# Performance work log

Hardware: AMD Instinct MI355X
Metric: run time of the kernel (lower is better)

## Reference

```python
import jax, jax.numpy as jnp
import numpy as np

ALPHA = 0.25
GAMMA = 2.0
HUBER_DELTA = 0.5  # init kwarg delta
REG_BETA = 1.0 / 9.0


def calc_iou(a, b):
    # a: [A,4] anchors, b: [M,4] gt boxes, xyxy
    area = (b[:, 2] - b[:, 0]) * (b[:, 3] - b[:, 1])  # [M]
    iw = jnp.clip(jnp.minimum(a[:, 2:3], b[:, 2]) - jnp.maximum(a[:, 0:1], b[:, 0]), 0.0)
    ih = jnp.clip(jnp.minimum(a[:, 3:4], b[:, 3]) - jnp.maximum(a[:, 1:2], b[:, 1]), 0.0)
    ua = jnp.clip(((a[:, 2] - a[:, 0]) * (a[:, 3] - a[:, 1]))[:, None] + area - iw * ih, 1e-8)
    return iw * ih / ua  # [A,M]


def _per_sample(cls, reg, dist, ann, anchor):
    # cls [A,C], reg [A,4], dist [A,1], ann [M,6], anchor [A,4]
    aw = anchor[:, 2] - anchor[:, 0]
    ah = anchor[:, 3] - anchor[:, 1]
    acx = anchor[:, 0] + 0.5 * aw
    acy = anchor[:, 1] + 0.5 * ah

    valid = ann[:, 4] != -1.0  # padding annotations have class == -1
    cls = jnp.clip(cls, 1e-4, 1.0 - 1e-4)

    iou = jnp.where(valid[None, :], calc_iou(anchor, ann[:, :4]), -1.0)  # [A,M]
    iou_max = iou.max(axis=1)
    iou_arg = iou.argmax(axis=1)
    assigned = ann[iou_arg]  # [A,6]

    pos = iou_max >= 0.5
    num_pos = pos.sum()
    denom = jnp.maximum(num_pos.astype(cls.dtype), 1.0)

    labels = assigned[:, 4].astype(jnp.int32)
    onehot = jax.nn.one_hot(labels, cls.shape[1], dtype=cls.dtype)
    # -1 = ignore, 0 = negative (IoU<0.4 or positive-but-not-this-class), 1 = assigned class
    targets = jnp.where(pos[:, None], onehot,
                        jnp.where((iou_max < 0.4)[:, None], 0.0, -1.0))

    af = jnp.where(targets == 1.0, ALPHA, 1.0 - ALPHA)
    fw = af * jnp.where(targets == 1.0, 1.0 - cls, cls) ** GAMMA
    bce = -(targets * jnp.log(cls) + (1.0 - targets) * jnp.log(1.0 - cls))
    cls_loss = jnp.where(targets != -1.0, fw * bce, 0.0).sum() / denom

    # empty-annotation fallback: all anchors treated as background
    cls_loss_empty = ((1.0 - ALPHA) * cls ** GAMMA * (-jnp.log(1.0 - cls))).sum()
    has_ann = valid.any()
    cls_loss = jnp.where(has_ann, cls_loss, cls_loss_empty)

    gw_raw = assigned[:, 2] - assigned[:, 0]
    gh_raw = assigned[:, 3] - assigned[:, 1]
    gcx = assigned[:, 0] + 0.5 * gw_raw  # centers use unclamped w/h (as in torch code)
    gcy = assigned[:, 1] + 0.5 * gh_raw
    gw = jnp.clip(gw_raw, 1.0)
    gh = jnp.clip(gh_raw, 1.0)
    t = jnp.stack([(gcx - acx) / aw, (gcy - acy) / ah,
                   jnp.log(gw / aw), jnp.log(gh / ah)], axis=1)
    t = t / jnp.asarray([0.1, 0.1, 0.2, 0.2], dtype=cls.dtype)
    diff = jnp.abs(t - reg)
    rl = jnp.where(diff <= REG_BETA, 0.5 * 9.0 * diff ** 2, diff - 0.5 / 9.0)
    posf = pos.astype(cls.dtype)
    reg_loss = jnp.where(num_pos > 0, (rl * posf[:, None]).sum() / (denom * 4.0), 0.0)

    # --- distance Huber loss (delta=0.5), positives only ---
    d = jnp.abs(dist[:, 0] - assigned[:, 5])
    hl = jnp.where(d <= HUBER_DELTA, 0.5 * d ** 2, HUBER_DELTA * (d - 0.5 * HUBER_DELTA))
    dist_loss = jnp.where(num_pos > 0, (hl * posf).sum() / denom, 0.0)

    return cls_loss, reg_loss, dist_loss


def reference(classifications, regressions, distances, anchors, annotations):
    anchor = anchors[0]
    cl, rl, dl = jax.vmap(_per_sample, in_axes=(0, 0, 0, 0, None))(
        classifications, regressions, distances, annotations, anchor)
    return (jnp.mean(cl, keepdims=True),
            jnp.mean(rl, keepdims=True),
            jnp.mean(dl, keepdims=True))


def setup_inputs() -> dict:
    key = jax.random.key(0)
    ks = jax.random.split(key, 10)
    B, A, C, M = 8, 120000, 80, 32
    IMG = 800.0

    classifications = jax.random.uniform(ks[0], (B, A, C), dtype=jnp.float32)
    regressions = jax.random.normal(ks[1], (B, A, 4), dtype=jnp.float32)
    distances = jax.random.normal(ks[2], (B, A, 1), dtype=jnp.float32) * 10.0 + 50.0

    # anchors: valid xyxy boxes over an 800px image
    acx = jax.random.uniform(ks[3], (A,), minval=0.0, maxval=IMG)
    acy = jax.random.uniform(ks[4], (A,), minval=0.0, maxval=IMG)
    aw = jax.random.uniform(ks[5], (A, 2), minval=16.0, maxval=256.0)
    anchors = jnp.stack([acx - 0.5 * aw[:, 0], acy - 0.5 * aw[:, 1],
                         acx + 0.5 * aw[:, 0], acy + 0.5 * aw[:, 1]], axis=1)[None].astype(jnp.float32)

    # annotations: [B,M,6] = x1,y1,x2,y2,class,distance (all valid)
    gc = jax.random.uniform(ks[6], (B, M, 2), minval=100.0, maxval=IMG - 100.0)
    gs = jax.random.uniform(ks[7], (B, M, 2), minval=32.0, maxval=300.0)
    boxes = jnp.concatenate([gc - 0.5 * gs, gc + 0.5 * gs], axis=-1)
    labels = jax.random.randint(ks[8], (B, M, 1), 0, C).astype(jnp.float32)
    gdist = jax.random.uniform(ks[9], (B, M, 1), minval=1.0, maxval=100.0)
    annotations = jnp.concatenate([boxes, labels, gdist], axis=-1).astype(jnp.float32)

    return {"classifications": classifications, "regressions": regressions,
            "distances": distances, "anchors": anchors, "annotations": annotations}
```

## Files before the change

### kernel.cpp

```cpp
#include <hip/hip_runtime.h>
#include <hip/hip_bf16.h>


typedef float v4f __attribute__((ext_vector_type(4)));

#define LN2_075 0.51986038542f

__device__ __forceinline__ float wave_reduce_sum(float v) {
#pragma unroll
    for (int off = 32; off > 0; off >>= 1) v += __shfl_down(v, off);
    return v;
}

__device__ __forceinline__ float smooth_l1(float d) {
    return d <= (1.0f / 9.0f) ? 4.5f * d * d : d - (0.5f / 9.0f);
}

template <int CPA>
__global__ __launch_bounds__(256) void fused_kernel(
    const float* __restrict__ cls, const float* __restrict__ reg,
    const float* __restrict__ dist, const float* __restrict__ anchors,
    const float* __restrict__ ann, float4* __restrict__ partials,
    int A, int M, int nb) {
    const int b = blockIdx.y;
    const int base = blockIdx.x << 8;
    const int tid = threadIdx.x;
    const int lane = tid & 63;

    __shared__ float s_ann[64 * 6];
    const float* annb = ann + (size_t)b * M * 6;
    for (int i = tid; i < M * 6; i += 256) s_ann[i] = annb[i];

    const v4f* __restrict__ clsb = (const v4f*)(cls + ((size_t)b * A + base) * (CPA * 4));
    float acc2 = 0.f;
    if (base + 256 <= A) {
#pragma unroll
        for (int k = 0; k < CPA; ++k) {
            const v4f cv = __builtin_nontemporal_load(&clsb[k * 256 + tid]);
#pragma unroll
            for (int j = 0; j < 4; ++j) {
                const float c = fminf(fmaxf(cv[j], 1e-4f), 1.0f - 1e-4f);
                acc2 = fmaf(c * c, __log2f(1.0f - c), acc2);
            }
        }
    } else {
        const int nch = (A - base) * CPA;
        for (int k = 0; k < CPA; ++k) {
            const int idx = k * 256 + tid;
            if (idx < nch) {
                const v4f cv = __builtin_nontemporal_load(&clsb[idx]);
#pragma unroll
                for (int j = 0; j < 4; ++j) {
                    const float c = fminf(fmaxf(cv[j], 1e-4f), 1.0f - 1e-4f);
                    acc2 = fmaf(c * c, __log2f(1.0f - c), acc2);
                }
            }
        }
    }

    __syncthreads();

    const int a = base + tid;
    float l_npos = 0.f, l_reg = 0.f, l_dist = 0.f;
    int st = -1;
    if (a < A) {
        const float4 av = *(const float4*)(anchors + (size_t)a * 4);
        const float aw = av.z - av.x, ah = av.w - av.y;
        const float acx = av.x + 0.5f * aw, acy = av.y + 0.5f * ah;
        const float aarea = aw * ah;

        float best = -1.0f;
        int bi = 0;
        for (int m = 0; m < M; ++m) {
            const float* g = s_ann + m * 6;
            float iou = -1.0f;
            if (g[4] != -1.0f) {
                float iw = fmaxf(fminf(av.z, g[2]) - fmaxf(av.x, g[0]), 0.f);
                float ih = fmaxf(fminf(av.w, g[3]) - fmaxf(av.y, g[1]), 0.f);
                float inter = iw * ih;
                float area = (g[2] - g[0]) * (g[3] - g[1]);
                float ua = fmaxf(aarea + area - inter, 1e-8f);
                iou = inter / ua;
            }
            if (iou > best) { best = iou; bi = m; }
        }

        if (best >= 0.5f) {
            const float* g = s_ann + bi * 6;
            st = (int)g[4];
            l_npos = 1.f;
            const float4 rv = *(const float4*)(reg + ((size_t)b * A + a) * 4);
            const float gwr = g[2] - g[0], ghr = g[3] - g[1];
            const float gcx = g[0] + 0.5f * gwr, gcy = g[1] + 0.5f * ghr;
            const float gw = fmaxf(gwr, 1.f), gh = fmaxf(ghr, 1.f);
            const float t0 = ((gcx - acx) / aw) / 0.1f;
            const float t1 = ((gcy - acy) / ah) / 0.1f;
            const float t2 = __logf(gw / aw) / 0.2f;
            const float t3 = __logf(gh / ah) / 0.2f;
            l_reg = smooth_l1(fabsf(t0 - rv.x)) + smooth_l1(fabsf(t1 - rv.y)) +
                    smooth_l1(fabsf(t2 - rv.z)) + smooth_l1(fabsf(t3 - rv.w));
            const float dv = dist[(size_t)b * A + a];
            const float dd = fabsf(dv - g[5]);
            l_dist = dd <= 0.5f ? 0.5f * dd * dd : 0.5f * (dd - 0.25f);
        } else if (best >= 0.4f) {
            st = -2;
        }
    }

    float corr = 0.f;
    unsigned long long mask = __ballot(st != -1);
    const int wbase = tid & ~63;
    while (mask) {
        const int bit = (int)__ffsll(mask) - 1;
        mask &= mask - 1;
        const int sst = __shfl(st, bit);
        const int la = wbase + bit;
        if (sst == -2) {
            float part = 0.f;
            if (lane < CPA) {
                const v4f cv = clsb[(size_t)la * CPA + lane];
#pragma unroll
                for (int j = 0; j < 4; ++j) {
                    const float c = fminf(fmaxf(cv[j], 1e-4f), 1.0f - 1e-4f);
                    part = fmaf(c * c, __log2f(1.0f - c), part);
                }
            }
            part = wave_reduce_sum(part);
            if (lane == 0) corr += LN2_075 * part;
        } else if (lane == 0) {
            const float cr = cls[((size_t)b * A + base + la) * (CPA * 4) + sst];
            const float c = fminf(fmaxf(cr, 1e-4f), 1.0f - 1e-4f);
            const float om = 1.0f - c;
            corr += LN2_075 * (c * c * __log2f(om))
                    + 0.25f * om * om * (-__logf(c));
        }
    }

    const float lsum = fmaf(acc2, -LN2_075, corr);

    __shared__ float s_red[4][4];
    const float w0 = wave_reduce_sum(l_npos);
    const float w1 = wave_reduce_sum(lsum);
    const float w2 = wave_reduce_sum(l_reg);
    const float w3 = wave_reduce_sum(l_dist);
    const int wid = tid >> 6;
    if (lane == 0) {
        s_red[0][wid] = w0; s_red[1][wid] = w1; s_red[2][wid] = w2; s_red[3][wid] = w3;
    }
    __syncthreads();
    if (tid == 0) {
        float4 p;
        p.x = s_red[0][0] + s_red[0][1] + s_red[0][2] + s_red[0][3];
        p.y = s_red[1][0] + s_red[1][1] + s_red[1][2] + s_red[1][3];
        p.z = s_red[2][0] + s_red[2][1] + s_red[2][2] + s_red[2][3];
        p.w = s_red[3][0] + s_red[3][1] + s_red[3][2] + s_red[3][3];
        partials[(size_t)b * nb + blockIdx.x] = p;
    }
}

__global__ void finalize_kernel(const float4* __restrict__ partials,
                                float* __restrict__ out, int B, int nb) {
    const int lane = threadIdx.x & 63;
    const int b = threadIdx.x >> 6;
    __shared__ float s_res[8][3];
    if (b < B) {
        float np_ = 0.f, cs = 0.f, rs = 0.f, ds = 0.f;
        for (int i = lane; i < nb; i += 64) {
            const float4 p = partials[(size_t)b * nb + i];
            np_ += p.x; cs += p.y; rs += p.z; ds += p.w;
        }
        np_ = wave_reduce_sum(np_);
        cs = wave_reduce_sum(cs);
        rs = wave_reduce_sum(rs);
        ds = wave_reduce_sum(ds);
        if (lane == 0) {
            const float denom = fmaxf(np_, 1.f);
            s_res[b][0] = cs / denom;
            s_res[b][1] = np_ > 0.f ? rs / (denom * 4.f) : 0.f;
            s_res[b][2] = np_ > 0.f ? ds / denom : 0.f;
        }
    }
    __syncthreads();
    if (threadIdx.x == 0) {
        float c = 0.f, r = 0.f, d = 0.f;
        for (int i = 0; i < B; ++i) { c += s_res[i][0]; r += s_res[i][1]; d += s_res[i][2]; }
        out[0] = c / (float)B;
        out[1] = r / (float)B;
        out[2] = d / (float)B;
    }
}

__global__ __launch_bounds__(256) void fused_generic_kernel(
    const float* __restrict__ cls, const float* __restrict__ reg,
    const float* __restrict__ dist, const float* __restrict__ anchors,
    const float* __restrict__ ann, float4* __restrict__ partials,
    int A, int C, int M, int nb) {
    const int b = blockIdx.y;
    const int base = blockIdx.x << 8;
    const int tid = threadIdx.x;
    const int cpa = C >> 2;

    __shared__ float s_ann[64 * 6];
    __shared__ signed char s_state[256];
    const float* annb = ann + (size_t)b * M * 6;
    for (int i = tid; i < M * 6; i += 256) s_ann[i] = annb[i];
    s_state[tid] = -2;
    __syncthreads();

    const int a = base + tid;
    float l_npos = 0.f, l_reg = 0.f, l_dist = 0.f;
    if (a < A) {
        const float4 av = *(const float4*)(anchors + (size_t)a * 4);
        const float aw = av.z - av.x, ah = av.w - av.y;
        const float acx = av.x + 0.5f * aw, acy = av.y + 0.5f * ah;
        const float aarea = aw * ah;
        float best = -1.0f;
        int bi = 0;
        for (int m = 0; m < M; ++m) {
            const float* g = s_ann + m * 6;
            float iou = -1.0f;
            if (g[4] != -1.0f) {
                float iw = fmaxf(fminf(av.z, g[2]) - fmaxf(av.x, g[0]), 0.f);
                float ih = fmaxf(fminf(av.w, g[3]) - fmaxf(av.y, g[1]), 0.f);
                float inter = iw * ih;
                float area = (g[2] - g[0]) * (g[3] - g[1]);
                float ua = fmaxf(aarea + area - inter, 1e-8f);
                iou = inter / ua;
            }
            if (iou > best) { best = iou; bi = m; }
        }
        signed char st;
        if (best >= 0.5f) {
            const float* g = s_ann + bi * 6;
            st = (signed char)(int)g[4];
            l_npos = 1.f;
            const float4 rv = *(const float4*)(reg + ((size_t)b * A + a) * 4);
            const float gwr = g[2] - g[0], ghr = g[3] - g[1];
            const float gcx = g[0] + 0.5f * gwr, gcy = g[1] + 0.5f * ghr;
            const float gw = fmaxf(gwr, 1.f), gh = fmaxf(ghr, 1.f);
            const float t0 = ((gcx - acx) / aw) / 0.1f;
            const float t1 = ((gcy - acy) / ah) / 0.1f;
            const float t2 = __logf(gw / aw) / 0.2f;
            const float t3 = __logf(gh / ah) / 0.2f;
            l_reg = smooth_l1(fabsf(t0 - rv.x)) + smooth_l1(fabsf(t1 - rv.y)) +
                    smooth_l1(fabsf(t2 - rv.z)) + smooth_l1(fabsf(t3 - rv.w));
            const float dv = dist[(size_t)b * A + a];
            const float dd = fabsf(dv - g[5]);
            l_dist = dd <= 0.5f ? 0.5f * dd * dd : 0.5f * (dd - 0.25f);
        } else if (best < 0.4f) {
            st = -1;
        } else {
            st = -2;
        }
        s_state[tid] = st;
    }
    __syncthreads();

    const float4* __restrict__ clsb = (const float4*)(cls + ((size_t)b * A + base) * C);
    int a_local = tid / cpa;
    int cc = tid % cpa;
    const int dA = 256 / cpa;
    const int dC = 256 % cpa;
    float lsum = 0.f;
    for (int k = 0; k < cpa; ++k) {
        const int st = s_state[a_local];
        if (st != -2) {
            const float4 cv = clsb[k * 256 + tid];
            const int c0 = cc << 2;
#pragma unroll
            for (int j = 0; j < 4; ++j) {
                float c = j == 0 ? cv.x : j == 1 ? cv.y : j == 2 ? cv.z : cv.w;
                c = fminf(fmaxf(c, 1e-4f), 1.0f - 1e-4f);
                const bool ispos = (st == c0 + j);
                const float om = 1.0f - c;
                const float x = ispos ? c : om;
                const float w = ispos ? 0.25f * om * om : 0.75f * c * c;
                lsum -= w * __logf(x);
            }
        }
        a_local += dA;
        cc += dC;
        if (cc >= cpa) { cc -= cpa; ++a_local; }
    }

    __shared__ float s_red[4][4];
    const float w0 = wave_reduce_sum(l_npos);
    const float w1 = wave_reduce_sum(lsum);
    const float w2 = wave_reduce_sum(l_reg);
    const float w3 = wave_reduce_sum(l_dist);
    const int lane = tid & 63, wid = tid >> 6;
    if (lane == 0) {
        s_red[0][wid] = w0; s_red[1][wid] = w1; s_red[2][wid] = w2; s_red[3][wid] = w3;
    }
    __syncthreads();
    if (tid == 0) {
        float4 p;
        p.x = s_red[0][0] + s_red[0][1] + s_red[0][2] + s_red[0][3];
        p.y = s_red[1][0] + s_red[1][1] + s_red[1][2] + s_red[1][3];
        p.z = s_red[2][0] + s_red[2][1] + s_red[2][2] + s_red[2][3];
        p.w = s_red[3][0] + s_red[3][1] + s_red[3][2] + s_red[3][3];
        partials[(size_t)b * nb + blockIdx.x] = p;
    }
}

extern "C" void kernel_launch(void* const* d_in, const int* in_sizes, int n_in,
                              void* d_out, int out_size, void* d_ws, size_t ws_size,
                              hipStream_t stream) {
    const float* cls     = (const float*)d_in[0];
    const float* reg     = (const float*)d_in[1];
    const float* dist    = (const float*)d_in[2];
    const float* anchors = (const float*)d_in[3];
    const float* ann     = (const float*)d_in[4];

    const int A = in_sizes[3] / 4;
    const int B = in_sizes[1] / (A * 4);
    const int C = in_sizes[0] / (B * A);
    const int M = in_sizes[4] / (B * 6);
    const int nb = (A + 255) / 256;

    float4* partials = (float4*)d_ws;

    dim3 g(nb, B), blk(256);
    if (C == 80) {
        fused_kernel<20><<<g, blk, 0, stream>>>(cls, reg, dist, anchors, ann,
                                                partials, A, M, nb);
    } else {
        fused_generic_kernel<<<g, blk, 0, stream>>>(cls, reg, dist, anchors, ann,
                                                    partials, A, C, M, nb);
    }
    finalize_kernel<<<1, B * 64, 0, stream>>>(partials, (float*)d_out, B, nb);
}
```

Before: 84.13 us.

## Split dense class-loss streaming into separate grid-stride blocks from anchor matching

The grid gains a fixed set of 256 streaming blocks per batch that grid-stride over the whole classification tensor with 4-way unrolled nontemporal loads. These blocks accumulate the background focal term. The remaining blocks do only IoU matching, the sparse correction terms and the regression and distance losses. The finalize kernel combines both partial arrays. The aim is to decouple the bandwidth-bound stream from the compute-heavy IoU loop and balance the load, at the cost of an extra partials buffer and a fixed block count that may not match the hardware.

```diff
diff --git a/kernel.cpp b/kernel.cpp
--- a/kernel.cpp
+++ b/kernel.cpp
@@ -16,48 +16,59 @@
     return d <= (1.0f / 9.0f) ? 4.5f * d * d : d - (0.5f / 9.0f);
 }
 
+__device__ __forceinline__ float proc4(v4f cv, float acc) {
+#pragma unroll
+    for (int j = 0; j < 4; ++j) {
+        const float c = fminf(fmaxf(cv[j], 1e-4f), 1.0f - 1e-4f);
+        acc = fmaf(c * c, __log2f(1.0f - c), acc);
+    }
+    return acc;
+}
+
 template <int CPA>
-__global__ __launch_bounds__(256) void fused_kernel(
+__global__ __launch_bounds__(256) void main_kernel(
     const float* __restrict__ cls, const float* __restrict__ reg,
     const float* __restrict__ dist, const float* __restrict__ anchors,
-    const float* __restrict__ ann, float4* __restrict__ partials,
-    int A, int M, int nb) {
+    const float* __restrict__ ann, float* __restrict__ partA,
+    float4* __restrict__ partB, int A, int M, int SBLK, int nb) {
     const int b = blockIdx.y;
-    const int base = blockIdx.x << 8;
     const int tid = threadIdx.x;
     const int lane = tid & 63;
+    const int wid = tid >> 6;
+
+    if (blockIdx.x < SBLK) {
+        const int NC4 = A * CPA;
+        const v4f* __restrict__ p = (const v4f*)(cls + (size_t)b * NC4 * 4);
+        const int s = SBLK << 8;
+        int i = (blockIdx.x << 8) + tid;
+        float acc = 0.f;
+        for (; i + 3 * s < NC4; i += 4 * s) {
+            const v4f a0 = __builtin_nontemporal_load(&p[i]);
+            const v4f a1 = __builtin_nontemporal_load(&p[i + s]);
+            const v4f a2 = __builtin_nontemporal_load(&p[i + 2 * s]);
+            const v4f a3 = __builtin_nontemporal_load(&p[i + 3 * s]);
+            acc = proc4(a0, acc);
+            acc = proc4(a1, acc);
+            acc = proc4(a2, acc);
+            acc = proc4(a3, acc);
+        }
+        for (; i < NC4; i += s) acc = proc4(__builtin_nontemporal_load(&p[i]), acc);
+
+        __shared__ float s_red[4];
+        acc = wave_reduce_sum(acc);
+        if (lane == 0) s_red[wid] = acc;
+        __syncthreads();
+        if (tid == 0)
+            partA[(size_t)b * SBLK + blockIdx.x] = s_red[0] + s_red[1] + s_red[2] + s_red[3];
+        return;
+    }
+
+    const int blk = blockIdx.x - SBLK;
+    const int base = blk << 8;
 
     __shared__ float s_ann[64 * 6];
     const float* annb = ann + (size_t)b * M * 6;
     for (int i = tid; i < M * 6; i += 256) s_ann[i] = annb[i];
-
-    const v4f* __restrict__ clsb = (const v4f*)(cls + ((size_t)b * A + base) * (CPA * 4));
-    float acc2 = 0.f;
-    if (base + 256 <= A) {
-#pragma unroll
-        for (int k = 0; k < CPA; ++k) {
-            const v4f cv = __builtin_nontemporal_load(&clsb[k * 256 + tid]);
-#pragma unroll
-            for (int j = 0; j < 4; ++j) {
-                const float c = fminf(fmaxf(cv[j], 1e-4f), 1.0f - 1e-4f);
-                acc2 = fmaf(c * c, __log2f(1.0f - c), acc2);
-            }
-        }
-    } else {
-        const int nch = (A - base) * CPA;
-        for (int k = 0; k < CPA; ++k) {
-            const int idx = k * 256 + tid;
-            if (idx < nch) {
-                const v4f cv = __builtin_nontemporal_load(&clsb[idx]);
-#pragma unroll
-                for (int j = 0; j < 4; ++j) {
-                    const float c = fminf(fmaxf(cv[j], 1e-4f), 1.0f - 1e-4f);
-                    acc2 = fmaf(c * c, __log2f(1.0f - c), acc2);
-                }
-            }
-        }
-    }
-
     __syncthreads();
 
     const int a = base + tid;
@@ -107,6 +118,7 @@
         }
     }
 
+    const v4f* __restrict__ clsb = (const v4f*)(cls + ((size_t)b * A + base) * (CPA * 4));
     float corr = 0.f;
     unsigned long long mask = __ballot(st != -1);
     const int wbase = tid & ~63;
@@ -119,11 +131,7 @@
             float part = 0.f;
             if (lane < CPA) {
                 const v4f cv = clsb[(size_t)la * CPA + lane];
-#pragma unroll
-                for (int j = 0; j < 4; ++j) {
-                    const float c = fminf(fmaxf(cv[j], 1e-4f), 1.0f - 1e-4f);
-                    part = fmaf(c * c, __log2f(1.0f - c), part);
-                }
+                part = proc4(cv, part);
             }
             part = wave_reduce_sum(part);
             if (lane == 0) corr += LN2_075 * part;
@@ -136,46 +144,47 @@
         }
     }
 
-    const float lsum = fmaf(acc2, -LN2_075, corr);
-
-    __shared__ float s_red[4][4];
+    __shared__ float s_red4[4][4];
     const float w0 = wave_reduce_sum(l_npos);
-    const float w1 = wave_reduce_sum(lsum);
+    const float w1 = wave_reduce_sum(corr);
     const float w2 = wave_reduce_sum(l_reg);
     const float w3 = wave_reduce_sum(l_dist);
-    const int wid = tid >> 6;
     if (lane == 0) {
-        s_red[0][wid] = w0; s_red[1][wid] = w1; s_red[2][wid] = w2; s_red[3][wid] = w3;
+        s_red4[0][wid] = w0; s_red4[1][wid] = w1; s_red4[2][wid] = w2; s_red4[3][wid] = w3;
     }
     __syncthreads();
     if (tid == 0) {
         float4 p;
-        p.x = s_red[0][0] + s_red[0][1] + s_red[0][2] + s_red[0][3];
-        p.y = s_red[1][0] + s_red[1][1] + s_red[1][2] + s_red[1][3];
-        p.z = s_red[2][0] + s_red[2][1] + s_red[2][2] + s_red[2][3];
-        p.w = s_red[3][0] + s_red[3][1] + s_red[3][2] + s_red[3][3];
-        partials[(size_t)b * nb + blockIdx.x] = p;
-    }
-}
-
-__global__ void finalize_kernel(const float4* __restrict__ partials,
-                                float* __restrict__ out, int B, int nb) {
+        p.x = s_red4[0][0] + s_red4[0][1] + s_red4[0][2] + s_red4[0][3];
+        p.y = s_red4[1][0] + s_red4[1][1] + s_red4[1][2] + s_red4[1][3];
+        p.z = s_red4[2][0] + s_red4[2][1] + s_red4[2][2] + s_red4[2][3];
+        p.w = s_red4[3][0] + s_red4[3][1] + s_red4[3][2] + s_red4[3][3];
+        partB[(size_t)b * nb + blk] = p;
+    }
+}
+
+__global__ void finalize_kernel(const float* __restrict__ partA,
+                                const float4* __restrict__ partB,
+                                float* __restrict__ out, int B, int SBLK, int nb) {
     const int lane = threadIdx.x & 63;
     const int b = threadIdx.x >> 6;
     __shared__ float s_res[8][3];
     if (b < B) {
-        float np_ = 0.f, cs = 0.f, rs = 0.f, ds = 0.f;
+        float sa = 0.f, np_ = 0.f, corr = 0.f, rs = 0.f, ds = 0.f;
+        for (int i = lane; i < SBLK; i += 64) sa += partA[(size_t)b * SBLK + i];
         for (int i = lane; i < nb; i += 64) {
-            const float4 p = partials[(size_t)b * nb + i];
-            np_ += p.x; cs += p.y; rs += p.z; ds += p.w;
-        }
+            const float4 p = partB[(size_t)b * nb + i];
+            np_ += p.x; corr += p.y; rs += p.z; ds += p.w;
+        }
+        sa = wave_reduce_sum(sa);
         np_ = wave_reduce_sum(np_);
-        cs = wave_reduce_sum(cs);
+        corr = wave_reduce_sum(corr);
         rs = wave_reduce_sum(rs);
         ds = wave_reduce_sum(ds);
         if (lane == 0) {
+            const float cls_total = fmaf(sa, -LN2_075, corr);
             const float denom = fmaxf(np_, 1.f);
-            s_res[b][0] = cs / denom;
+            s_res[b][0] = cls_total / denom;
             s_res[b][1] = np_ > 0.f ? rs / (denom * 4.f) : 0.f;
             s_res[b][2] = np_ > 0.f ? ds / denom : 0.f;
         }
@@ -317,16 +326,20 @@
     const int C = in_sizes[0] / (B * A);
     const int M = in_sizes[4] / (B * 6);
     const int nb = (A + 255) / 256;
-
-    float4* partials = (float4*)d_ws;
-
-    dim3 g(nb, B), blk(256);
+    const int SBLK = 256;
+
+    float* partA = (float*)d_ws;
+    float4* partB = (float4*)((char*)d_ws + 8192);
+
     if (C == 80) {
-        fused_kernel<20><<<g, blk, 0, stream>>>(cls, reg, dist, anchors, ann,
-                                                partials, A, M, nb);
+        dim3 g(SBLK + nb, B), blk(256);
+        main_kernel<20><<<g, blk, 0, stream>>>(cls, reg, dist, anchors, ann,
+                                               partA, partB, A, M, SBLK, nb);
+        finalize_kernel<<<1, B * 64, 0, stream>>>(partA, partB, (float*)d_out, B, SBLK, nb);
     } else {
+        dim3 g(nb, B), blk(256);
         fused_generic_kernel<<<g, blk, 0, stream>>>(cls, reg, dist, anchors, ann,
-                                                    partials, A, C, M, nb);
-    }
-    finalize_kernel<<<1, B * 64, 0, stream>>>(partials, (float*)d_out, B, nb);
-}
+                                                    partB, A, C, M, nb);
+        finalize_kernel<<<1, B * 64, 0, stream>>>(partA, partB, (float*)d_out, B, 0, nb);
+    }
+}
```

New measurement: 79.43 us. 5.6% less time.
